# Performance work log

Hardware: AMD Instinct MI355X
Metric: run time of the kernel (lower is better)

The kernel has to match this reference:

```python
import jax, jax.numpy as jnp
import numpy as np


def setup_inputs() -> dict:
    key = jax.random.key(0)
    k1, k2, k3, k4 = jax.random.split(key, 4)
    B, S, D, R = 8, 1024, 1024, 256
    batch = jax.random.normal(k1, (B, S, D), dtype=jnp.float32)
    proj_L = jax.random.uniform(k2, (D, R), dtype=jnp.float32, minval=-0.05, maxval=0.05)
    proj_R = jax.random.uniform(k3, (R, D), dtype=jnp.float32, minval=-0.05, maxval=0.05)
    bias = jax.random.uniform(k4, (1,), dtype=jnp.float32, minval=-0.05, maxval=0.05)
    return {"batch": batch, "proj_L": proj_L, "proj_R": proj_R, "bias": bias}


def reference(batch, proj_L, proj_R, bias):
    # logits[b,i,j] = h_i^T (L @ R) h_j + bias
    # Efficient factored form (same math, avoids O(B*S^2*D) intermediates):
    # left[b,i,r] = (batch @ L)[b,i,r]; right[b,j,r] = (batch @ R^T)[b,j,r]
    left = jnp.einsum('bid,dr->bir', batch, proj_L)    # (B,S,R)
    right = jnp.einsum('bjd,rd->bjr', batch, proj_R)   # (B,S,R)
    logits = jnp.einsum('bir,bjr->bij', left, right) + bias[0]
    return logits
```

## Files before the change

kernel.cpp:

```cpp
#include <hip/hip_runtime.h>

typedef __bf16 bf16_t;
typedef __bf16 bf16x8 __attribute__((ext_vector_type(8)));
typedef __bf16 bf16x4 __attribute__((ext_vector_type(4)));
typedef float f32x4 __attribute__((ext_vector_type(4)));

__device__ __forceinline__ void async16(const void* g, void* l) {
  __builtin_amdgcn_global_load_lds(
      (const __attribute__((address_space(1))) unsigned int*)g,
      (__attribute__((address_space(3))) unsigned int*)l,
      16, 0, 0);
}

__global__ void convert_f32_bf16(const float* __restrict__ in,
                                 bf16_t* __restrict__ out, int n4) {
  int i = blockIdx.x * blockDim.x + threadIdx.x;
  if (i >= n4) return;
  float4 v = ((const float4*)in)[i];
  bf16x4 o;
  o[0] = (bf16_t)v.x; o[1] = (bf16_t)v.y; o[2] = (bf16_t)v.z; o[3] = (bf16_t)v.w;
  ((bf16x4*)out)[i] = o;
}

__global__ void prep_Bcat(const float* __restrict__ projL,
                          const float* __restrict__ projR,
                          bf16_t* __restrict__ Bcat) {
  const int t = threadIdx.x;
  if (blockIdx.x < 256) {
    int i = blockIdx.x * 256 + t;
    float4 v = ((const float4*)projR)[i];
    bf16x4 o;
    o[0] = (bf16_t)v.x; o[1] = (bf16_t)v.y; o[2] = (bf16_t)v.z; o[3] = (bf16_t)v.w;
    ((bf16x4*)(Bcat + (long)256 * 1024))[i] = o;
  } else {
    __shared__ float tile[32][33];
    const int bb = blockIdx.x - 256;
    const int n0 = (bb & 7) * 32;
    const int k0 = (bb >> 3) * 32;
    const int tx = t & 31;
    const int ty = t >> 5;
#pragma unroll
    for (int i = 0; i < 32; i += 8)
      tile[ty + i][tx] = projL[(long)(k0 + ty + i) * 256 + n0 + tx];
    __syncthreads();
#pragma unroll
    for (int i = 0; i < 32; i += 8)
      Bcat[(long)(n0 + ty + i) * 1024 + k0 + tx] = (bf16_t)tile[tx][ty + i];
  }
}

template <bool BF16_OUT>
__global__ __launch_bounds__(256) void gemm_bt(
    const bf16_t* __restrict__ A0, long sA, int lda,
    const bf16_t* __restrict__ B0, long sB, int ldb,
    void* __restrict__ C0, long sC, int ldc,
    int K, int tilesN, const float* __restrict__ bias) {
  const int bz = blockIdx.y;
  const bf16_t* A = A0 + (long)bz * sA;
  const bf16_t* Bt = B0 + (long)bz * sB;
  const int tm = (int)(blockIdx.x / tilesN) * 128;
  const int tn = (int)(blockIdx.x % tilesN) * 128;

  __shared__ __attribute__((aligned(16))) bf16_t As[4 * 128 * 32];
  __shared__ __attribute__((aligned(16))) bf16_t Bs[4 * 128 * 32];

  const int t = threadIdx.x;
  const int lane = t & 63;
  const int quad = lane >> 4;
  const int l15 = lane & 15;
  const int wave = t >> 6;
  const int wr = (wave >> 1) * 64;
  const int wc = (wave & 1) * 64;

  const int rS = t >> 2;
  const int cS = (t & 3) * 8;
  const bf16_t* gA = A + (long)(tm + rS) * lda + cS;
  const bf16_t* gB = Bt + (long)(tn + rS) * ldb + cS;
  bf16_t* lA = As + t * 8;
  bf16_t* lB = Bs + t * 8;

  f32x4 acc[4][4];
#pragma unroll
  for (int i = 0; i < 4; ++i)
#pragma unroll
    for (int j = 0; j < 4; ++j)
      acc[i][j] = (f32x4){0.f, 0.f, 0.f, 0.f};

  for (int k0 = 0; k0 < K; k0 += 128) {
#pragma unroll
    for (int kc = 0; kc < 4; ++kc) {
      const int ko = k0 + kc * 32;
      const int lo = kc * 4096;
      async16(gA + ko, lA + lo);
      async16(gA + ko + (long)64 * lda, lA + lo + 2048);
      async16(gB + ko, lB + lo);
      async16(gB + ko + (long)64 * ldb, lB + lo + 2048);
    }
    __syncthreads();

#pragma unroll
    for (int kc = 0; kc < 4; ++kc) {
      const bf16_t* Ak = As + kc * 4096;
      const bf16_t* Bk = Bs + kc * 4096;
      bf16x8 af[4], bv[4];
#pragma unroll
      for (int i = 0; i < 4; ++i)
        af[i] = *(const bf16x8*)(Ak + (wr + i * 16 + l15) * 32 + quad * 8);
#pragma unroll
      for (int j = 0; j < 4; ++j)
        bv[j] = *(const bf16x8*)(Bk + (wc + j * 16 + l15) * 32 + quad * 8);
#pragma unroll
      for (int i = 0; i < 4; ++i)
#pragma unroll
        for (int j = 0; j < 4; ++j)
          acc[i][j] = __builtin_amdgcn_mfma_f32_16x16x32_bf16(af[i], bv[j],
                                                              acc[i][j], 0, 0, 0);
    }
    __syncthreads();
  }

  if constexpr (BF16_OUT) {
    bf16_t* C = (bf16_t*)C0 + (long)bz * sC;
#pragma unroll
    for (int i = 0; i < 4; ++i) {
      const int r0 = tm + wr + i * 16 + quad * 4;
#pragma unroll
      for (int j = 0; j < 4; ++j) {
        const int c0 = tn + wc + j * 16 + l15;
#pragma unroll
        for (int r = 0; r < 4; ++r)
          C[(long)(r0 + r) * ldc + c0] = (bf16_t)acc[i][j][r];
      }
    }
  } else {
    float* C = (float*)C0 + (long)bz * sC;
    const float bvadd = bias[0];
#pragma unroll
    for (int i = 0; i < 4; ++i) {
      const int r0 = tm + wr + i * 16 + quad * 4;
#pragma unroll
      for (int j = 0; j < 4; ++j) {
        const int c0 = tn + wc + j * 16 + l15;
#pragma unroll
        for (int r = 0; r < 4; ++r)
          C[(long)(r0 + r) * ldc + c0] = acc[i][j][r] + bvadd;
      }
    }
  }
}

extern "C" void kernel_launch(void* const* d_in, const int* in_sizes, int n_in,
                              void* d_out, int out_size, void* d_ws,
                              size_t ws_size, hipStream_t stream) {
  const float* batch = (const float*)d_in[0];
  const float* projL = (const float*)d_in[1];
  const float* projR = (const float*)d_in[2];
  const float* bias = (const float*)d_in[3];
  float* out = (float*)d_out;

  constexpr int B = 8, S = 1024, D = 1024, R = 256;
  constexpr long nBatch = (long)B * S * D;

  char* ws = (char*)d_ws;
  bf16_t* batch_bf = (bf16_t*)ws;
  bf16_t* Bcat = (bf16_t*)(ws + nBatch * 2);
  bf16_t* LR = (bf16_t*)(ws + nBatch * 2 + (long)512 * 1024 * 2);

  convert_f32_bf16<<<(int)(nBatch / 4 + 255) / 256, 256, 0, stream>>>(
      batch, batch_bf, (int)(nBatch / 4));
  prep_Bcat<<<512, 256, 0, stream>>>(projL, projR, Bcat);

  gemm_bt<true><<<dim3(64 * 4, 1), 256, 0, stream>>>(
      batch_bf, 0L, D, Bcat, 0L, D, (void*)LR, 0L, 512, D, 4, nullptr);

  gemm_bt<false><<<dim3(8 * 8, 8), 256, 0, stream>>>(
      LR, (long)S * 512, 512, LR + 256, (long)S * 512, 512, (void*)out,
      (long)S * S, S, R, 8, bias);
}
```

Baseline: 123.0 us.

## Fuse fp32-to-bf16 conversion into GEMM and double-buffer the K loop

Removes the standalone conversion kernel for the input batch; the first GEMM now loads fp32 rows directly, converts them to bf16 in registers and writes them to shared memory. The K loop becomes a two-stage double-buffered pipeline with 64-wide stages, prefetching the next stage while computing the current one with a single barrier per iteration. This cuts a full extra read/write pass over the large input but adds register pressure and relies on the barrier covering the async LDS loads.

```diff
diff --git a/kernel.cpp b/kernel.cpp
--- a/kernel.cpp
+++ b/kernel.cpp
@@ -10,16 +10,6 @@
       (const __attribute__((address_space(1))) unsigned int*)g,
       (__attribute__((address_space(3))) unsigned int*)l,
       16, 0, 0);
-}
-
-__global__ void convert_f32_bf16(const float* __restrict__ in,
-                                 bf16_t* __restrict__ out, int n4) {
-  int i = blockIdx.x * blockDim.x + threadIdx.x;
-  if (i >= n4) return;
-  float4 v = ((const float4*)in)[i];
-  bf16x4 o;
-  o[0] = (bf16_t)v.x; o[1] = (bf16_t)v.y; o[2] = (bf16_t)v.z; o[3] = (bf16_t)v.w;
-  ((bf16x4*)out)[i] = o;
 }
 
 __global__ void prep_Bcat(const float* __restrict__ projL,
@@ -49,20 +39,19 @@
   }
 }
 
-template <bool BF16_OUT>
+template <bool A_FP32, bool BF16_OUT>
 __global__ __launch_bounds__(256) void gemm_bt(
-    const bf16_t* __restrict__ A0, long sA, int lda,
+    const void* __restrict__ A0v, long sA, int lda,
     const bf16_t* __restrict__ B0, long sB, int ldb,
     void* __restrict__ C0, long sC, int ldc,
     int K, int tilesN, const float* __restrict__ bias) {
   const int bz = blockIdx.y;
-  const bf16_t* A = A0 + (long)bz * sA;
   const bf16_t* Bt = B0 + (long)bz * sB;
   const int tm = (int)(blockIdx.x / tilesN) * 128;
   const int tn = (int)(blockIdx.x % tilesN) * 128;
 
-  __shared__ __attribute__((aligned(16))) bf16_t As[4 * 128 * 32];
-  __shared__ __attribute__((aligned(16))) bf16_t Bs[4 * 128 * 32];
+  __shared__ __attribute__((aligned(16))) bf16_t As[2 * 2 * 4096];
+  __shared__ __attribute__((aligned(16))) bf16_t Bs[2 * 2 * 4096];
 
   const int t = threadIdx.x;
   const int lane = t & 63;
@@ -74,10 +63,15 @@
 
   const int rS = t >> 2;
   const int cS = (t & 3) * 8;
-  const bf16_t* gA = A + (long)(tm + rS) * lda + cS;
   const bf16_t* gB = Bt + (long)(tn + rS) * ldb + cS;
-  bf16_t* lA = As + t * 8;
-  bf16_t* lB = Bs + t * 8;
+
+  const bf16_t* gA16 = nullptr;
+  const float* gA32 = nullptr;
+  if constexpr (A_FP32) {
+    gA32 = (const float*)A0v + (long)(tm + (t >> 3)) * lda + (t & 7) * 8;
+  } else {
+    gA16 = (const bf16_t*)A0v + (long)bz * sA + (long)(tm + rS) * lda + cS;
+  }
 
   f32x4 acc[4][4];
 #pragma unroll
@@ -86,22 +80,70 @@
     for (int j = 0; j < 4; ++j)
       acc[i][j] = (f32x4){0.f, 0.f, 0.f, 0.f};
 
-  for (int k0 = 0; k0 < K; k0 += 128) {
-#pragma unroll
-    for (int kc = 0; kc < 4; ++kc) {
-      const int ko = k0 + kc * 32;
-      const int lo = kc * 4096;
-      async16(gA + ko, lA + lo);
-      async16(gA + ko + (long)64 * lda, lA + lo + 2048);
-      async16(gB + ko, lB + lo);
-      async16(gB + ko + (long)64 * ldb, lB + lo + 2048);
-    }
+  const int NS = K >> 6;
+  float4 fa[4], fb[4];
+
+  auto stageB = [&](int buf, int ko) {
+    const bf16_t* g = gB + ko;
+    bf16_t* l = Bs + buf * 8192 + t * 8;
+    async16(g, l);
+    async16(g + (long)64 * ldb, l + 2048);
+    async16(g + 32, l + 4096);
+    async16(g + 32 + (long)64 * ldb, l + 6144);
+  };
+  auto stageA16 = [&](int buf, int ko) {
+    const bf16_t* g = gA16 + ko;
+    bf16_t* l = As + buf * 8192 + t * 8;
+    async16(g, l);
+    async16(g + (long)64 * lda, l + 2048);
+    async16(g + 32, l + 4096);
+    async16(g + 32 + (long)64 * lda, l + 6144);
+  };
+  auto loadA32 = [&](int ko) {
+#pragma unroll
+    for (int i = 0; i < 4; ++i) {
+      const float* p = gA32 + ko + (long)32 * i * lda;
+      fa[i] = *(const float4*)p;
+      fb[i] = *(const float4*)(p + 4);
+    }
+  };
+  auto writeA32 = [&](int buf) {
+    const int sub = (t & 7) >> 2;
+    const int cin = ((t & 7) & 3) * 8;
+#pragma unroll
+    for (int i = 0; i < 4; ++i) {
+      bf16x8 v;
+      v[0] = (bf16_t)fa[i].x; v[1] = (bf16_t)fa[i].y;
+      v[2] = (bf16_t)fa[i].z; v[3] = (bf16_t)fa[i].w;
+      v[4] = (bf16_t)fb[i].x; v[5] = (bf16_t)fb[i].y;
+      v[6] = (bf16_t)fb[i].z; v[7] = (bf16_t)fb[i].w;
+      *(bf16x8*)(As + buf * 8192 + sub * 4096 + ((t >> 3) + 32 * i) * 32 + cin) = v;
+    }
+  };
+
+  if constexpr (A_FP32) {
+    loadA32(0);
+    writeA32(0);
+  } else {
+    stageA16(0, 0);
+  }
+  stageB(0, 0);
+
+  for (int s = 0; s < NS; ++s) {
+    const int cur = s & 1;
     __syncthreads();
 
-#pragma unroll
-    for (int kc = 0; kc < 4; ++kc) {
-      const bf16_t* Ak = As + kc * 4096;
-      const bf16_t* Bk = Bs + kc * 4096;
+    const bool pf = (s + 1 < NS);
+    if (pf) {
+      if constexpr (A_FP32) loadA32((s + 1) * 64);
+      else stageA16(cur ^ 1, (s + 1) * 64);
+      stageB(cur ^ 1, (s + 1) * 64);
+    }
+
+#pragma unroll
+    for (int kc = 0; kc < 2; ++kc) {
+      const bf16_t* Ak = As + cur * 8192 + kc * 4096;
+      const bf16_t* Bk = Bs + cur * 8192 + kc * 4096;
       bf16x8 af[4], bv[4];
 #pragma unroll
       for (int i = 0; i < 4; ++i)
@@ -116,7 +158,10 @@
           acc[i][j] = __builtin_amdgcn_mfma_f32_16x16x32_bf16(af[i], bv[j],
                                                               acc[i][j], 0, 0, 0);
     }
-    __syncthreads();
+
+    if (pf) {
+      if constexpr (A_FP32) writeA32(cur ^ 1);
+    }
   }
 
   if constexpr (BF16_OUT) {
@@ -158,22 +203,19 @@
   const float* bias = (const float*)d_in[3];
   float* out = (float*)d_out;
 
-  constexpr int B = 8, S = 1024, D = 1024, R = 256;
-  constexpr long nBatch = (long)B * S * D;
+  constexpr int S = 1024, D = 1024, R = 256;
 
   char* ws = (char*)d_ws;
-  bf16_t* batch_bf = (bf16_t*)ws;
-  bf16_t* Bcat = (bf16_t*)(ws + nBatch * 2);
-  bf16_t* LR = (bf16_t*)(ws + nBatch * 2 + (long)512 * 1024 * 2);
-
-  convert_f32_bf16<<<(int)(nBatch / 4 + 255) / 256, 256, 0, stream>>>(
-      batch, batch_bf, (int)(nBatch / 4));
+  bf16_t* Bcat = (bf16_t*)ws;
+  bf16_t* LR = (bf16_t*)(ws + (long)512 * 1024 * 2);
+
   prep_Bcat<<<512, 256, 0, stream>>>(projL, projR, Bcat);
 
-  gemm_bt<true><<<dim3(64 * 4, 1), 256, 0, stream>>>(
-      batch_bf, 0L, D, Bcat, 0L, D, (void*)LR, 0L, 512, D, 4, nullptr);
-
-  gemm_bt<false><<<dim3(8 * 8, 8), 256, 0, stream>>>(
-      LR, (long)S * 512, 512, LR + 256, (long)S * 512, 512, (void*)out,
-      (long)S * S, S, R, 8, bias);
-}
+  gemm_bt<true, true><<<dim3(64 * 4, 1), 256, 0, stream>>>(
+      (const void*)batch, 0L, D, Bcat, 0L, D, (void*)LR, 0L, 512, D, 4,
+      nullptr);
+
+  gemm_bt<false, false><<<dim3(8 * 8, 8), 256, 0, stream>>>(
+      (const void*)LR, (long)S * 512, 512, LR + 256, (long)S * 512, 512,
+      (void*)out, (long)S * S, S, R, 8, bias);
+}
```

Measured after the change: 124.3 us. Within noise of the previous version (+1.1%).

## Fuse f32-to-bf16 conversion of batch into the first GEMM's A-tile loads

Applied to the files above, without the earlier changes.

Removes the separate conversion kernel and the bf16 copy of the batch tensor by having the first GEMM load f32 rows directly, convert in registers, and store bf16 into shared memory. The second GEMM is specialised with constant sizes and strides. This saves a kernel launch and the write and re-read of the converted intermediate. The cost is synchronous A loads instead of async LDS copies, and the f32 A tiles are read once per N tile.

```diff
diff --git a/kernel.cpp b/kernel.cpp
--- a/kernel.cpp
+++ b/kernel.cpp
@@ -10,16 +10,6 @@
       (const __attribute__((address_space(1))) unsigned int*)g,
       (__attribute__((address_space(3))) unsigned int*)l,
       16, 0, 0);
-}
-
-__global__ void convert_f32_bf16(const float* __restrict__ in,
-                                 bf16_t* __restrict__ out, int n4) {
-  int i = blockIdx.x * blockDim.x + threadIdx.x;
-  if (i >= n4) return;
-  float4 v = ((const float4*)in)[i];
-  bf16x4 o;
-  o[0] = (bf16_t)v.x; o[1] = (bf16_t)v.y; o[2] = (bf16_t)v.z; o[3] = (bf16_t)v.w;
-  ((bf16x4*)out)[i] = o;
 }
 
 __global__ void prep_Bcat(const float* __restrict__ projL,
@@ -49,20 +39,15 @@
   }
 }
 
-template <bool BF16_OUT>
-__global__ __launch_bounds__(256) void gemm_bt(
-    const bf16_t* __restrict__ A0, long sA, int lda,
-    const bf16_t* __restrict__ B0, long sB, int ldb,
-    void* __restrict__ C0, long sC, int ldc,
-    int K, int tilesN, const float* __restrict__ bias) {
-  const int bz = blockIdx.y;
-  const bf16_t* A = A0 + (long)bz * sA;
-  const bf16_t* Bt = B0 + (long)bz * sB;
-  const int tm = (int)(blockIdx.x / tilesN) * 128;
-  const int tn = (int)(blockIdx.x % tilesN) * 128;
-
-  __shared__ __attribute__((aligned(16))) bf16_t As[4 * 128 * 32];
-  __shared__ __attribute__((aligned(16))) bf16_t Bs[4 * 128 * 32];
+__global__ __launch_bounds__(256, 1) void gemm1_fusedA(
+    const float* __restrict__ batch, const bf16_t* __restrict__ Bcat,
+    bf16_t* __restrict__ LR) {
+  const int bx = blockIdx.x;
+  const int tm = (bx & 63) * 128;
+  const int tn = (bx >> 6) * 128;
+
+  __shared__ __attribute__((aligned(16))) bf16_t As[4 * 4096];
+  __shared__ __attribute__((aligned(16))) bf16_t Bs[4 * 4096];
 
   const int t = threadIdx.x;
   const int lane = t & 63;
@@ -74,10 +59,13 @@
 
   const int rS = t >> 2;
   const int cS = (t & 3) * 8;
-  const bf16_t* gA = A + (long)(tm + rS) * lda + cS;
-  const bf16_t* gB = Bt + (long)(tn + rS) * ldb + cS;
-  bf16_t* lA = As + t * 8;
+  const bf16_t* gB = Bcat + (long)(tn + rS) * 1024 + cS;
   bf16_t* lB = Bs + t * 8;
+
+  const int rA = t >> 4;
+  const int cA = (t & 15) * 8;
+  const float* gA = batch + (long)(tm + rA) * 1024 + cA;
+  bf16_t* lA = As + (cA >> 5) * 4096 + (cA & 31);
 
   f32x4 acc[4][4];
 #pragma unroll
@@ -86,15 +74,28 @@
     for (int j = 0; j < 4; ++j)
       acc[i][j] = (f32x4){0.f, 0.f, 0.f, 0.f};
 
-  for (int k0 = 0; k0 < K; k0 += 128) {
-#pragma unroll
-    for (int kc = 0; kc < 4; ++kc) {
-      const int ko = k0 + kc * 32;
-      const int lo = kc * 4096;
-      async16(gA + ko, lA + lo);
-      async16(gA + ko + (long)64 * lda, lA + lo + 2048);
-      async16(gB + ko, lB + lo);
-      async16(gB + ko + (long)64 * ldb, lB + lo + 2048);
+  for (int s = 0; s < 8; ++s) {
+    const int k0 = s * 128;
+#pragma unroll
+    for (int kc = 0; kc < 4; ++kc) {
+      async16(gB + k0 + kc * 32, lB + kc * 4096);
+      async16(gB + k0 + kc * 32 + (long)64 * 1024, lB + kc * 4096 + 2048);
+    }
+    float4 fa[8], fb[8];
+#pragma unroll
+    for (int i = 0; i < 8; ++i) {
+      const float* p = gA + k0 + (long)16 * i * 1024;
+      fa[i] = *(const float4*)p;
+      fb[i] = *(const float4*)(p + 4);
+    }
+#pragma unroll
+    for (int i = 0; i < 8; ++i) {
+      bf16x8 v;
+      v[0] = (bf16_t)fa[i].x; v[1] = (bf16_t)fa[i].y;
+      v[2] = (bf16_t)fa[i].z; v[3] = (bf16_t)fa[i].w;
+      v[4] = (bf16_t)fb[i].x; v[5] = (bf16_t)fb[i].y;
+      v[6] = (bf16_t)fb[i].z; v[7] = (bf16_t)fb[i].w;
+      *(bf16x8*)(lA + (rA + 16 * i) * 32) = v;
     }
     __syncthreads();
 
@@ -119,32 +120,98 @@
     __syncthreads();
   }
 
-  if constexpr (BF16_OUT) {
-    bf16_t* C = (bf16_t*)C0 + (long)bz * sC;
-#pragma unroll
-    for (int i = 0; i < 4; ++i) {
-      const int r0 = tm + wr + i * 16 + quad * 4;
-#pragma unroll
-      for (int j = 0; j < 4; ++j) {
-        const int c0 = tn + wc + j * 16 + l15;
-#pragma unroll
-        for (int r = 0; r < 4; ++r)
-          C[(long)(r0 + r) * ldc + c0] = (bf16_t)acc[i][j][r];
-      }
-    }
-  } else {
-    float* C = (float*)C0 + (long)bz * sC;
-    const float bvadd = bias[0];
-#pragma unroll
-    for (int i = 0; i < 4; ++i) {
-      const int r0 = tm + wr + i * 16 + quad * 4;
-#pragma unroll
-      for (int j = 0; j < 4; ++j) {
-        const int c0 = tn + wc + j * 16 + l15;
-#pragma unroll
-        for (int r = 0; r < 4; ++r)
-          C[(long)(r0 + r) * ldc + c0] = acc[i][j][r] + bvadd;
-      }
+#pragma unroll
+  for (int i = 0; i < 4; ++i) {
+    const int r0 = tm + wr + i * 16 + quad * 4;
+#pragma unroll
+    for (int j = 0; j < 4; ++j) {
+      const int c0 = tn + wc + j * 16 + l15;
+#pragma unroll
+      for (int r = 0; r < 4; ++r)
+        LR[(long)(r0 + r) * 512 + c0] = (bf16_t)acc[i][j][r];
+    }
+  }
+}
+
+__global__ __launch_bounds__(256) void gemm2(const bf16_t* __restrict__ LR,
+                                             float* __restrict__ out,
+                                             const float* __restrict__ bias) {
+  const int bz = blockIdx.y;
+  const int bx = blockIdx.x;
+  const int tm = (bx & 7) * 128;
+  const int tn = (bx >> 3) * 128;
+  const bf16_t* LRb = LR + (long)bz * 1024 * 512;
+
+  __shared__ __attribute__((aligned(16))) bf16_t As[4 * 4096];
+  __shared__ __attribute__((aligned(16))) bf16_t Bs[4 * 4096];
+
+  const int t = threadIdx.x;
+  const int lane = t & 63;
+  const int quad = lane >> 4;
+  const int l15 = lane & 15;
+  const int wave = t >> 6;
+  const int wr = (wave >> 1) * 64;
+  const int wc = (wave & 1) * 64;
+
+  const int rS = t >> 2;
+  const int cS = (t & 3) * 8;
+  const bf16_t* gA = LRb + (long)(tm + rS) * 512 + cS;
+  const bf16_t* gB = LRb + (long)(tn + rS) * 512 + 256 + cS;
+  bf16_t* lA = As + t * 8;
+  bf16_t* lB = Bs + t * 8;
+
+  f32x4 acc[4][4];
+#pragma unroll
+  for (int i = 0; i < 4; ++i)
+#pragma unroll
+    for (int j = 0; j < 4; ++j)
+      acc[i][j] = (f32x4){0.f, 0.f, 0.f, 0.f};
+
+#pragma unroll
+  for (int s = 0; s < 2; ++s) {
+    const int k0 = s * 128;
+#pragma unroll
+    for (int kc = 0; kc < 4; ++kc) {
+      const int ko = k0 + kc * 32;
+      async16(gA + ko, lA + kc * 4096);
+      async16(gA + ko + (long)64 * 512, lA + kc * 4096 + 2048);
+      async16(gB + ko, lB + kc * 4096);
+      async16(gB + ko + (long)64 * 512, lB + kc * 4096 + 2048);
+    }
+    __syncthreads();
+
+#pragma unroll
+    for (int kc = 0; kc < 4; ++kc) {
+      const bf16_t* Ak = As + kc * 4096;
+      const bf16_t* Bk = Bs + kc * 4096;
+      bf16x8 af[4], bv[4];
+#pragma unroll
+      for (int i = 0; i < 4; ++i)
+        af[i] = *(const bf16x8*)(Ak + (wr + i * 16 + l15) * 32 + quad * 8);
+#pragma unroll
+      for (int j = 0; j < 4; ++j)
+        bv[j] = *(const bf16x8*)(Bk + (wc + j * 16 + l15) * 32 + quad * 8);
+#pragma unroll
+      for (int i = 0; i < 4; ++i)
+#pragma unroll
+        for (int j = 0; j < 4; ++j)
+          acc[i][j] = __builtin_amdgcn_mfma_f32_16x16x32_bf16(af[i], bv[j],
+                                                              acc[i][j], 0, 0, 0);
+    }
+    __syncthreads();
+  }
+
+  float* C = out + (long)bz * 1024 * 1024;
+  const float bvadd = bias[0];
+#pragma unroll
+  for (int i = 0; i < 4; ++i) {
+    const int r0 = tm + wr + i * 16 + quad * 4;
+#pragma unroll
+    for (int j = 0; j < 4; ++j) {
+      const int c0 = tn + wc + j * 16 + l15;
+#pragma unroll
+      for (int r = 0; r < 4; ++r)
+        C[(long)(r0 + r) * 1024 + c0] = acc[i][j][r] + bvadd;
     }
   }
 }
@@ -158,22 +225,13 @@
   const float* bias = (const float*)d_in[3];
   float* out = (float*)d_out;
 
-  constexpr int B = 8, S = 1024, D = 1024, R = 256;
-  constexpr long nBatch = (long)B * S * D;
-
   char* ws = (char*)d_ws;
-  bf16_t* batch_bf = (bf16_t*)ws;
-  bf16_t* Bcat = (bf16_t*)(ws + nBatch * 2);
-  bf16_t* LR = (bf16_t*)(ws + nBatch * 2 + (long)512 * 1024 * 2);
-
-  convert_f32_bf16<<<(int)(nBatch / 4 + 255) / 256, 256, 0, stream>>>(
-      batch, batch_bf, (int)(nBatch / 4));
+  bf16_t* Bcat = (bf16_t*)ws;
+  bf16_t* LR = (bf16_t*)(ws + (long)512 * 1024 * 2);
+
   prep_Bcat<<<512, 256, 0, stream>>>(projL, projR, Bcat);
 
-  gemm_bt<true><<<dim3(64 * 4, 1), 256, 0, stream>>>(
-      batch_bf, 0L, D, Bcat, 0L, D, (void*)LR, 0L, 512, D, 4, nullptr);
-
-  gemm_bt<false><<<dim3(8 * 8, 8), 256, 0, stream>>>(
-      LR, (long)S * 512, 512, LR + 256, (long)S * 512, 512, (void*)out,
-      (long)S * S, S, R, 8, bias);
-}
+  gemm1_fusedA<<<256, 256, 0, stream>>>(batch, Bcat, LR);
+
+  gemm2<<<dim3(64, 8), 256, 0, stream>>>(LR, out, bias);
+}
```

Result: faster. 117.7 us (-4.3%).
